# Kernel tuning notes

Hardware: AMD Instinct MI355X
Metric: run time of the kernel (lower is better)

Reference implementation:

```python
import jax, jax.numpy as jnp
import numpy as np


def setup_inputs() -> dict:
    key = jax.random.key(0)
    k_x, k_idx, k_sgn = jax.random.split(key, 3)
    batch, original_dim, proj_dim, c = 32, 1000000, 4096, 8
    x = jax.random.normal(k_x, (batch, original_dim), dtype=jnp.float32)
    rand_indices = jax.random.randint(k_idx, (original_dim, c), 0, proj_dim, dtype=jnp.int32)
    # random signs in {-1, +1}, matching torch.randint(0,2)*2-1 cast to int8
    rand_signs = (jax.random.randint(k_sgn, (original_dim, c), 0, 2, dtype=jnp.int32) * 2 - 1)
    return {"x": x, "rand_indices": rand_indices, "rand_signs": rand_signs,
            "proj_dim": proj_dim, "c": c}


def reference(x, rand_indices, rand_signs, proj_dim, c):
    # SJLT: each input coordinate d is scattered to c random output buckets
    # with random sign; normalized by 1/sqrt(c) so the sketch preserves norms.
    scale = jnp.asarray(1.0 / np.sqrt(c), dtype=x.dtype)
    batch = x.shape[0]
    out = jnp.zeros((batch, proj_dim), dtype=x.dtype)
    # c is a small fixed constant; loop over it, vectorize over batch & features.
    for j in range(c):
        vals = x * rand_signs[:, j].astype(x.dtype)      # [B, D]
        out = out.at[:, rand_indices[:, j]].add(vals)     # scatter-add along proj dim
    return out * scale
```

## Files before the change

### kernel.cpp

```cpp
#include <hip/hip_runtime.h>
#include <hip/hip_fp16.h>


#define D_TOTAL 1000000
#define PROJ    4096
#define C_SK    8
#define NE      (D_TOTAL * C_SK)
#define SCALE   0.35355339059327373f

#define NSEG    16
#define SEG_D   62500
#define CAPA2   8448
#define BINCAP_A 96
#define CAPH    96
#define TILE    4096
#define NBLK_A  ((NE + TILE - 1) / TILE)
#define NBLK_T  ((D_TOTAL + 255) / 256)
#define NSLICE  (NSEG * 2)

#define SMEM_FUSED 25088

#define CURA_OFF   0
#define XT_OFF     16384
#define XT_SZ      ((size_t)D_TOTAL * 32 * 2)
#define LISTA_OFF  (XT_OFF + XT_SZ)
#define LISTA_SZ   ((size_t)NSEG * 64 * CAPA2 * 4)
#define PART_OFF   (LISTA_OFF + LISTA_SZ)
#define PART_SZ    ((size_t)NSLICE * PROJ * 32 * 4)
#define WS_NEED    (PART_OFF + PART_SZ)

__global__ void init_cursors_kernel(int* __restrict__ curA) {
    int i = blockIdx.x * blockDim.x + threadIdx.x;
    if (i < NSEG * 64) curA[i] = i * CAPA2;
}

template<int BC>
__device__ __forceinline__ void rank_and_stage(bool ok, int kb, int payload,
                                               int* __restrict__ cnt,
                                               int* __restrict__ stage,
                                               int* __restrict__ gcur,
                                               int* __restrict__ glist,
                                               int gcur_idx, int glim) {
    if (ok) {
        const int pos = atomicAdd(&cnt[kb], 1);
        if (pos < BC) {
            stage[kb * BC + pos] = payload;
        } else {
            const int gp = atomicAdd(&gcur[gcur_idx], 1);
            if (gp < glim) glist[gp] = payload;
        }
    }
}

template<int BC>
__device__ __forceinline__ void flush_bins(int* __restrict__ cnt,
                                           int* __restrict__ basek,
                                           const int* __restrict__ stage,
                                           int* __restrict__ gcur,
                                           int* __restrict__ glist,
                                           int gidx0, int capPer) {
    const int tid = threadIdx.x;
    if (tid < 64) {
        const int m = min(cnt[tid], BC);
        cnt[tid]   = m;
        basek[tid] = atomicAdd(&gcur[gidx0 + tid], m);
    }
    __syncthreads();
    const int w = tid >> 6, lane = tid & 63;
    #pragma unroll 1
    for (int bi = 0; bi < 16; ++bi) {
        const int kb  = w * 16 + bi;
        const int m   = cnt[kb];
        const int gb  = basek[kb];
        const int lim = (gidx0 + kb + 1) * capPer;
        for (int i = lane; i < m; i += 64)
            if (gb + i < lim) glist[gb + i] = stage[kb * BC + i];
    }
}

__device__ __forceinline__ void pass_a_body(int abid, char* smem,
                                            const int* __restrict__ idx,
                                            const int* __restrict__ sgn,
                                            int* __restrict__ curA,
                                            int* __restrict__ listA) {
    int* stage = (int*)smem;
    int* cnt   = (int*)(smem + 64 * BINCAP_A * 4);
    int* basek = cnt + 64;
    const int tid = threadIdx.x;
    if (tid < 64) cnt[tid] = 0;
    __syncthreads();

    const int d_lo = abid * 512;
    const int seg  = d_lo / SEG_D;
    const bool boundary = ((d_lo + 511) / SEG_D) != seg;
    const int v0 = abid * (TILE / 4);

    #pragma unroll 1
    for (int k = 0; k < TILE / 1024; ++k) {
        const int vi = v0 + k * 256 + tid;
        const bool okv = vi < NE / 4;
        int4 i4 = {0,0,0,0}, s4 = {0,0,0,0};
        if (okv) { i4 = ((const int4*)idx)[vi]; s4 = ((const int4*)sgn)[vi]; }
        const int g0 = vi * 4;
        #pragma unroll
        for (int m = 0; m < 4; ++m) {
            const int bucket = (m == 0) ? i4.x : (m == 1) ? i4.y : (m == 2) ? i4.z : i4.w;
            const int sg     = (m == 0) ? s4.x : (m == 1) ? s4.y : (m == 2) ? s4.z : s4.w;
            const int kb = okv ? (bucket >> 6) : 0;
            const int payload = (g0 + m) | ((bucket & 63) << 24)
                              | (int)((unsigned)sg & 0x80000000u);
            if (!boundary) {
                rank_and_stage<BINCAP_A>(okv, kb, payload, cnt, stage, curA, listA,
                                         seg * 64 + kb, (seg * 64 + kb + 1) * CAPA2);
            } else if (okv) {
                const int segE = ((g0 + m) >> 3) / SEG_D;
                const int bin  = segE * 64 + kb;
                const int gp = atomicAdd(&curA[bin], 1);
                if (gp < (bin + 1) * CAPA2) listA[gp] = payload;
            }
        }
    }
    __syncthreads();
    flush_bins<BINCAP_A>(cnt, basek, stage, curA, listA, seg * 64, CAPA2);
}

__device__ __forceinline__ void transpose_body(int tbid, char* smem,
                                               const float* __restrict__ x,
                                               unsigned short* __restrict__ xT) {
    unsigned short (*tile)[260] = (unsigned short(*)[260])smem;
    const int tid = threadIdx.x;
    const int d0  = tbid * 256;
    const int row = tid >> 3;
    const int c8  = tid & 7;

    if (d0 + 256 <= D_TOTAL) {
        #pragma unroll
        for (int k = 0; k < 8; ++k) {
            const int c = (c8 + 8 * k) * 4;
            const float4 v = *(const float4*)(x + (size_t)row * D_TOTAL + d0 + c);
            unsigned short h[4];
            h[0] = __half_as_ushort(__float2half(v.x));
            h[1] = __half_as_ushort(__float2half(v.y));
            h[2] = __half_as_ushort(__float2half(v.z));
            h[3] = __half_as_ushort(__float2half(v.w));
            *(uint2*)&tile[row][c] = *(const uint2*)h;
        }
    } else {
        for (int k = 0; k < 8; ++k) {
            const int c = (c8 + 8 * k) * 4;
            for (int m = 0; m < 4; ++m) {
                const int d = d0 + c + m;
                tile[row][c + m] = __half_as_ushort(
                    __float2half((d < D_TOTAL) ? x[(size_t)row * D_TOTAL + d] : 0.f));
            }
        }
    }
    __syncthreads();

    const int part = tid & 3;
    #pragma unroll
    for (int k = 0; k < 4; ++k) {
        const int dl = k * 64 + (tid >> 2);
        if (d0 + dl < D_TOTAL) {
            unsigned short h[8];
            #pragma unroll
            for (int i = 0; i < 8; ++i)
                h[i] = tile[part * 8 + i][dl];
            *(uint4*)(xT + ((size_t)(d0 + dl)) * 32 + part * 8) = *(const uint4*)h;
        }
    }
}

__global__ __launch_bounds__(256, 6)
void pass_a_transpose_kernel(const int* __restrict__ idx, const int* __restrict__ sgn,
                             int* __restrict__ curA, int* __restrict__ listA,
                             const float* __restrict__ x, unsigned short* __restrict__ xT) {
    __shared__ char smem[SMEM_FUSED];
    const int id = blockIdx.x;
    if ((id % 3 == 0) && (id / 3 < NBLK_A)) {
        pass_a_body(id / 3, smem, idx, sgn, curA, listA);
    } else {
        const int tbid = id - id / 3 - ((id % 3) ? 1 : 0);
        if (tbid < NBLK_T) transpose_body(tbid, smem, x, xT);
    }
}

__global__ __launch_bounds__(256, 6)
void gather_part_kernel(const int* __restrict__ curA, const int* __restrict__ listA,
                        const unsigned short* __restrict__ xT,
                        float* __restrict__ partial, float* __restrict__ out) {
    __shared__ int stage[64 * CAPH];
    __shared__ int cnt[64];
    const int tid = threadIdx.x;
    const int gid = blockIdx.x;
    const int seg  = (gid & 7) + 8 * (gid >> 10);
    const int rest = (gid >> 3) & 127;
    const int kbA  = rest >> 1;
    const int half = rest & 1;
    const int part = seg * 64 + kbA;

    if (tid < 64) cnt[tid] = 0;
    __syncthreads();

    const int pstart = part * CAPA2;
    const int pcount = min(curA[part] - pstart, CAPA2);
    const int hn = (pcount + 1) >> 1;
    const int t0 = half * hn;
    const int t1 = min(t0 + hn, pcount);

    for (int i = t0 + tid; i < t1; i += 256) {
        const int e  = listA[pstart + i];
        const int kb = (e >> 24) & 63;
        const int pos = atomicAdd(&cnt[kb], 1);
        if (pos < CAPH) {
            stage[kb * CAPH + pos] = e;
        } else {
            int d = (e & 0x7FFFFF) >> 3;
            d = min(d, D_TOTAL - 1);
            const float s = (e < 0) ? -SCALE : SCALE;
            const int p = kbA * 64 + kb;
            for (int b = 0; b < 32; ++b) {
                const float v = __half2float(*(const __half*)(xT + (size_t)d * 32 + b));
                unsafeAtomicAdd(out + (size_t)b * PROJ + p, s * v);
            }
        }
    }
    __syncthreads();

    const int w    = tid >> 6;
    const int lane = tid & 63;
    const int slot = lane >> 2;
    const int bq   = lane & 3;
    #pragma unroll 1
    for (int bi = 0; bi < 16; ++bi) {
        const int kb = w * 16 + bi;
        const int n  = min(cnt[kb], CAPH);
        float a0=0.f,a1=0.f,a2=0.f,a3=0.f,a4=0.f,a5=0.f,a6=0.f,a7=0.f;
        #pragma unroll 2
        for (int base = 0; base < n; base += 16) {
            const int  e  = base + slot;
            const bool ok = e < n;
            const int  pl = stage[kb * CAPH + (ok ? e : 0)];
            int d = (pl & 0x7FFFFF) >> 3;
            d = min(d, D_TOTAL - 1);
            const float s = ok ? ((pl < 0) ? -1.f : 1.f) : 0.f;
            const uint4 hv = *(const uint4*)(xT + (size_t)d * 32 + bq * 8);
            float2 f;
            f = __half22float2(*(const __half2*)&hv.x); a0 = fmaf(s, f.x, a0); a1 = fmaf(s, f.y, a1);
            f = __half22float2(*(const __half2*)&hv.y); a2 = fmaf(s, f.x, a2); a3 = fmaf(s, f.y, a3);
            f = __half22float2(*(const __half2*)&hv.z); a4 = fmaf(s, f.x, a4); a5 = fmaf(s, f.y, a5);
            f = __half22float2(*(const __half2*)&hv.w); a6 = fmaf(s, f.x, a6); a7 = fmaf(s, f.y, a7);
        }
        #pragma unroll
        for (int m = 4; m <= 32; m <<= 1) {
            a0 += __shfl_xor(a0, m, 64); a1 += __shfl_xor(a1, m, 64);
            a2 += __shfl_xor(a2, m, 64); a3 += __shfl_xor(a3, m, 64);
            a4 += __shfl_xor(a4, m, 64); a5 += __shfl_xor(a5, m, 64);
            a6 += __shfl_xor(a6, m, 64); a7 += __shfl_xor(a7, m, 64);
        }
        if (lane < 4) {
            float v[8] = {a0,a1,a2,a3,a4,a5,a6,a7};
            const size_t slice = (size_t)(seg * 2 + half);
            float* dst = partial + (slice * PROJ + (size_t)(kbA * 64 + kb)) * 32 + lane * 8;
            #pragma unroll
            for (int i = 0; i < 8; ++i) dst[i] = v[i];
        }
    }
}

__global__ __launch_bounds__(256)
void reduce_kernel(const float* __restrict__ partial, float* __restrict__ out) {
    const int gtid = blockIdx.x * 256 + threadIdx.x;
    const int p = gtid & (PROJ - 1);
    const int b = gtid >> 12;
    float s = 0.f;
    #pragma unroll
    for (int sg = 0; sg < NSLICE; ++sg)
        s += partial[((size_t)(sg * PROJ + p)) * 32 + b];
    const size_t o = (size_t)b * PROJ + p;
    out[o] = out[o] + s * SCALE;
}

#define BG 8
#define NCHUNK 64
#define BLOCK 1024
__global__ __launch_bounds__(BLOCK, 4)
void sjlt_scatter_fallback(const float* __restrict__ x,
                           const int* __restrict__ idx,
                           const int* __restrict__ sgn,
                           float* __restrict__ out) {
    __shared__ float acc[BG * PROJ];
    const int tid = threadIdx.x;
    #pragma unroll
    for (int i = 0; i < (BG * PROJ) / BLOCK; ++i) acc[i * BLOCK + tid] = 0.0f;
    __syncthreads();
    const int chunk = D_TOTAL / NCHUNK;
    const int d0 = blockIdx.x * chunk;
    const int d1 = d0 + chunk;
    const int bg = blockIdx.y * BG;
    for (int d = d0 + tid; d < d1; d += BLOCK) {
        const int4 i0 = *(const int4*)(idx + (size_t)d * C_SK);
        const int4 i1 = *(const int4*)(idx + (size_t)d * C_SK + 4);
        const int4 s0 = *(const int4*)(sgn + (size_t)d * C_SK);
        const int4 s1 = *(const int4*)(sgn + (size_t)d * C_SK + 4);
        #pragma unroll
        for (int b = 0; b < BG; ++b) {
            const float xv = __builtin_nontemporal_load(x + (size_t)(bg + b) * D_TOTAL + d);
            const unsigned xb = __float_as_uint(xv);
            float* accb = acc + b * PROJ;
            atomicAdd(accb + i0.x, __uint_as_float(xb ^ ((unsigned)s0.x & 0x80000000u)));
            atomicAdd(accb + i0.y, __uint_as_float(xb ^ ((unsigned)s0.y & 0x80000000u)));
            atomicAdd(accb + i0.z, __uint_as_float(xb ^ ((unsigned)s0.z & 0x80000000u)));
            atomicAdd(accb + i0.w, __uint_as_float(xb ^ ((unsigned)s0.w & 0x80000000u)));
            atomicAdd(accb + i1.x, __uint_as_float(xb ^ ((unsigned)s1.x & 0x80000000u)));
            atomicAdd(accb + i1.y, __uint_as_float(xb ^ ((unsigned)s1.y & 0x80000000u)));
            atomicAdd(accb + i1.z, __uint_as_float(xb ^ ((unsigned)s1.z & 0x80000000u)));
            atomicAdd(accb + i1.w, __uint_as_float(xb ^ ((unsigned)s1.w & 0x80000000u)));
        }
    }
    __syncthreads();
    #pragma unroll
    for (int i = 0; i < (BG * PROJ) / BLOCK; ++i) {
        const int lin = i * BLOCK + tid;
        const int b = lin >> 12;
        const int pp = lin & (PROJ - 1);
        unsafeAtomicAdd(out + (size_t)(bg + b) * PROJ + pp, acc[lin] * SCALE);
    }
}

extern "C" void kernel_launch(void* const* d_in, const int* in_sizes, int n_in,
                              void* d_out, int out_size, void* d_ws, size_t ws_size,
                              hipStream_t stream) {
    const float* x   = (const float*)d_in[0];
    const int*   idx = (const int*)d_in[1];
    const int*   sgn = (const int*)d_in[2];
    float*       out = (float*)d_out;

    if (ws_size < WS_NEED) {
        (void)hipMemsetAsync(out, 0, (size_t)out_size * sizeof(float), stream);
        dim3 grid(NCHUNK, 32 / BG);
        sjlt_scatter_fallback<<<grid, BLOCK, 0, stream>>>(x, idx, sgn, out);
        return;
    }

    char* ws = (char*)d_ws;
    int*            curA    = (int*)(ws + CURA_OFF);
    unsigned short* xT      = (unsigned short*)(ws + XT_OFF);
    int*            listA   = (int*)(ws + LISTA_OFF);
    float*          partial = (float*)(ws + PART_OFF);

    (void)hipMemsetAsync(out, 0, (size_t)out_size * sizeof(float), stream);
    init_cursors_kernel<<<4, 256, 0, stream>>>(curA);
    pass_a_transpose_kernel<<<NBLK_A + NBLK_T, 256, 0, stream>>>(
        idx, sgn, curA, listA, x, xT);
    gather_part_kernel<<<2048, 256, 0, stream>>>(curA, listA, xT, partial, out);
    reduce_kernel<<<(32 * PROJ) / 256, 256, 0, stream>>>(partial, out);
}
```

Measured before the change: 370.4 us.

## Split fused pass-A/transpose kernel and rewrite transpose with swizzled LDS tile

Replaces the interleaved pass_a/transpose kernel with two separate launches, so each kernel gets its own shared-memory size and occupancy bound. The transpose is rewritten so each thread loads eight float4 rows directly into registers, converts them to half, and writes them into a compact XOR-swizzled LDS tile. It then reads back 8-byte chunks to emit 16-byte xT stores. This is meant to cut LDS bank conflicts and the larger shared footprint, at the cost of losing overlap between the binning and transpose work in one launch.

```diff
diff --git a/kernel.cpp b/kernel.cpp
--- a/kernel.cpp
+++ b/kernel.cpp
@@ -18,7 +18,7 @@
 #define NBLK_T  ((D_TOTAL + 255) / 256)
 #define NSLICE  (NSEG * 2)
 
-#define SMEM_FUSED 25088
+#define SMEM_A  25088
 
 #define CURA_OFF   0
 #define XT_OFF     16384
@@ -124,64 +124,67 @@
     flush_bins<BINCAP_A>(cnt, basek, stage, curA, listA, seg * 64, CAPA2);
 }
 
-__device__ __forceinline__ void transpose_body(int tbid, char* smem,
-                                               const float* __restrict__ x,
-                                               unsigned short* __restrict__ xT) {
-    unsigned short (*tile)[260] = (unsigned short(*)[260])smem;
-    const int tid = threadIdx.x;
-    const int d0  = tbid * 256;
-    const int row = tid >> 3;
-    const int c8  = tid & 7;
-
-    if (d0 + 256 <= D_TOTAL) {
-        #pragma unroll
-        for (int k = 0; k < 8; ++k) {
-            const int c = (c8 + 8 * k) * 4;
-            const float4 v = *(const float4*)(x + (size_t)row * D_TOTAL + d0 + c);
-            unsigned short h[4];
-            h[0] = __half_as_ushort(__float2half(v.x));
-            h[1] = __half_as_ushort(__float2half(v.y));
-            h[2] = __half_as_ushort(__float2half(v.z));
-            h[3] = __half_as_ushort(__float2half(v.w));
-            *(uint2*)&tile[row][c] = *(const uint2*)h;
-        }
+__global__ __launch_bounds__(256, 6)
+void pass_a_kernel(const int* __restrict__ idx, const int* __restrict__ sgn,
+                   int* __restrict__ curA, int* __restrict__ listA) {
+    __shared__ char smem[SMEM_A];
+    pass_a_body(blockIdx.x, smem, idx, sgn, curA, listA);
+}
+
+__global__ __launch_bounds__(256, 8)
+void transpose_kernel(const float* __restrict__ x, unsigned short* __restrict__ xT) {
+    __shared__ __align__(16) unsigned short tile[256 * 36];
+    const int tid = threadIdx.x;
+    const int d0  = blockIdx.x * 256;
+    const int o   = tid & 3;
+    const int dq  = tid >> 2;
+    const int dbase = d0 + dq * 4;
+
+    float4 v[8];
+    if (dbase + 4 <= D_TOTAL) {
+        #pragma unroll
+        for (int j = 0; j < 8; ++j)
+            v[j] = *(const float4*)(x + (size_t)(o * 8 + j) * D_TOTAL + dbase);
     } else {
-        for (int k = 0; k < 8; ++k) {
-            const int c = (c8 + 8 * k) * 4;
-            for (int m = 0; m < 4; ++m) {
-                const int d = d0 + c + m;
-                tile[row][c + m] = __half_as_ushort(
-                    __float2half((d < D_TOTAL) ? x[(size_t)row * D_TOTAL + d] : 0.f));
-            }
-        }
-    }
-    __syncthreads();
-
-    const int part = tid & 3;
+        #pragma unroll
+        for (int j = 0; j < 8; ++j) {
+            v[j].x = v[j].y = v[j].z = v[j].w = 0.f;
+            const float* row = x + (size_t)(o * 8 + j) * D_TOTAL;
+            if (dbase + 0 < D_TOTAL) v[j].x = row[dbase + 0];
+            if (dbase + 1 < D_TOTAL) v[j].y = row[dbase + 1];
+            if (dbase + 2 < D_TOTAL) v[j].z = row[dbase + 2];
+            if (dbase + 3 < D_TOTAL) v[j].w = row[dbase + 3];
+        }
+    }
+
+    const int s = dq & 7;
+    #pragma unroll
+    for (int m = 0; m < 4; ++m) {
+        unsigned short h[8];
+        #pragma unroll
+        for (int j = 0; j < 8; ++j) {
+            const float f = (m == 0) ? v[j].x : (m == 1) ? v[j].y
+                          : (m == 2) ? v[j].z : v[j].w;
+            h[j] = __half_as_ushort(__float2half(f));
+        }
+        const int row = dq * 4 + m;
+        unsigned short* rbase = &tile[row * 36];
+        *(uint2*)(rbase + (((2 * o + 0) ^ s) << 2)) = *(const uint2*)&h[0];
+        *(uint2*)(rbase + (((2 * o + 1) ^ s) << 2)) = *(const uint2*)&h[4];
+    }
+    __syncthreads();
+
     #pragma unroll
     for (int k = 0; k < 4; ++k) {
         const int dl = k * 64 + (tid >> 2);
         if (d0 + dl < D_TOTAL) {
-            unsigned short h[8];
-            #pragma unroll
-            for (int i = 0; i < 8; ++i)
-                h[i] = tile[part * 8 + i][dl];
-            *(uint4*)(xT + ((size_t)(d0 + dl)) * 32 + part * 8) = *(const uint4*)h;
-        }
-    }
-}
-
-__global__ __launch_bounds__(256, 6)
-void pass_a_transpose_kernel(const int* __restrict__ idx, const int* __restrict__ sgn,
-                             int* __restrict__ curA, int* __restrict__ listA,
-                             const float* __restrict__ x, unsigned short* __restrict__ xT) {
-    __shared__ char smem[SMEM_FUSED];
-    const int id = blockIdx.x;
-    if ((id % 3 == 0) && (id / 3 < NBLK_A)) {
-        pass_a_body(id / 3, smem, idx, sgn, curA, listA);
-    } else {
-        const int tbid = id - id / 3 - ((id % 3) ? 1 : 0);
-        if (tbid < NBLK_T) transpose_body(tbid, smem, x, xT);
+            const int s2 = (dl >> 2) & 7;
+            const unsigned short* rbase = &tile[dl * 36];
+            const uint2 r0 = *(const uint2*)(rbase + (((2 * o + 0) ^ s2) << 2));
+            const uint2 r1 = *(const uint2*)(rbase + (((2 * o + 1) ^ s2) << 2));
+            uint4 w; w.x = r0.x; w.y = r0.y; w.z = r1.x; w.w = r1.y;
+            *(uint4*)(xT + (size_t)(d0 + dl) * 32 + o * 8) = w;
+        }
     }
 }
 
@@ -217,11 +220,11 @@
         } else {
             int d = (e & 0x7FFFFF) >> 3;
             d = min(d, D_TOTAL - 1);
-            const float s = (e < 0) ? -SCALE : SCALE;
+            const float sgf = (e < 0) ? -SCALE : SCALE;
             const int p = kbA * 64 + kb;
             for (int b = 0; b < 32; ++b) {
-                const float v = __half2float(*(const __half*)(xT + (size_t)d * 32 + b));
-                unsafeAtomicAdd(out + (size_t)b * PROJ + p, s * v);
+                const float vv = __half2float(*(const __half*)(xT + (size_t)d * 32 + b));
+                unsafeAtomicAdd(out + (size_t)b * PROJ + p, sgf * vv);
             }
         }
     }
@@ -243,13 +246,13 @@
             const int  pl = stage[kb * CAPH + (ok ? e : 0)];
             int d = (pl & 0x7FFFFF) >> 3;
             d = min(d, D_TOTAL - 1);
-            const float s = ok ? ((pl < 0) ? -1.f : 1.f) : 0.f;
+            const float sg = ok ? ((pl < 0) ? -1.f : 1.f) : 0.f;
             const uint4 hv = *(const uint4*)(xT + (size_t)d * 32 + bq * 8);
             float2 f;
-            f = __half22float2(*(const __half2*)&hv.x); a0 = fmaf(s, f.x, a0); a1 = fmaf(s, f.y, a1);
-            f = __half22float2(*(const __half2*)&hv.y); a2 = fmaf(s, f.x, a2); a3 = fmaf(s, f.y, a3);
-            f = __half22float2(*(const __half2*)&hv.z); a4 = fmaf(s, f.x, a4); a5 = fmaf(s, f.y, a5);
-            f = __half22float2(*(const __half2*)&hv.w); a6 = fmaf(s, f.x, a6); a7 = fmaf(s, f.y, a7);
+            f = __half22float2(*(const __half2*)&hv.x); a0 = fmaf(sg, f.x, a0); a1 = fmaf(sg, f.y, a1);
+            f = __half22float2(*(const __half2*)&hv.y); a2 = fmaf(sg, f.x, a2); a3 = fmaf(sg, f.y, a3);
+            f = __half22float2(*(const __half2*)&hv.z); a4 = fmaf(sg, f.x, a4); a5 = fmaf(sg, f.y, a5);
+            f = __half22float2(*(const __half2*)&hv.w); a6 = fmaf(sg, f.x, a6); a7 = fmaf(sg, f.y, a7);
         }
         #pragma unroll
         for (int m = 4; m <= 32; m <<= 1) {
@@ -259,11 +262,11 @@
             a6 += __shfl_xor(a6, m, 64); a7 += __shfl_xor(a7, m, 64);
         }
         if (lane < 4) {
-            float v[8] = {a0,a1,a2,a3,a4,a5,a6,a7};
+            float vv[8] = {a0,a1,a2,a3,a4,a5,a6,a7};
             const size_t slice = (size_t)(seg * 2 + half);
             float* dst = partial + (slice * PROJ + (size_t)(kbA * 64 + kb)) * 32 + lane * 8;
             #pragma unroll
-            for (int i = 0; i < 8; ++i) dst[i] = v[i];
+            for (int i = 0; i < 8; ++i) dst[i] = vv[i];
         }
     }
 }
@@ -277,8 +280,8 @@
     #pragma unroll
     for (int sg = 0; sg < NSLICE; ++sg)
         s += partial[((size_t)(sg * PROJ + p)) * 32 + b];
-    const size_t o = (size_t)b * PROJ + p;
-    out[o] = out[o] + s * SCALE;
+    const size_t oidx = (size_t)b * PROJ + p;
+    out[oidx] = out[oidx] + s * SCALE;
 }
 
 #define BG 8
@@ -351,8 +354,8 @@
 
     (void)hipMemsetAsync(out, 0, (size_t)out_size * sizeof(float), stream);
     init_cursors_kernel<<<4, 256, 0, stream>>>(curA);
-    pass_a_transpose_kernel<<<NBLK_A + NBLK_T, 256, 0, stream>>>(
-        idx, sgn, curA, listA, x, xT);
+    pass_a_kernel<<<NBLK_A, 256, 0, stream>>>(idx, sgn, curA, listA);
+    transpose_kernel<<<NBLK_T, 256, 0, stream>>>(x, xT);
     gather_part_kernel<<<2048, 256, 0, stream>>>(curA, listA, xT, partial, out);
     reduce_kernel<<<(32 * PROJ) / 256, 256, 0, stream>>>(partial, out);
 }
```

Result: no change. 367.3 us (-0.8%).
